# Optimization experiments

Hardware: AMD Instinct MI355X
Metric: run time of the kernel (lower is better)

The kernel has to match this reference:

```python
import jax, jax.numpy as jnp
import numpy as np

SIGMA = 1.0

def _pairwise_sqdist(x, y):
    # x: [N,3], y: [M,3] -> [N,M] squared distances via gram expansion
    xx = jnp.sum(x * x, axis=-1)[:, None]
    yy = jnp.sum(y * y, axis=-1)[None, :]
    xy = x @ y.T
    return jnp.maximum(xx + yy - 2.0 * xy, 0.0)

def _cauchy(d2, sigma):
    return 1.0 / (1.0 + d2 / (sigma * sigma))

def setup_inputs() -> dict:
    key = jax.random.key(0)
    k1, k2, k3, k4 = jax.random.split(key, 4)
    V, N, M = 4096, 8192, 8192
    src_vertices = jax.random.normal(k1, (V, 3), dtype=jnp.float32)
    tar_normals = jax.random.normal(k2, (M, 3), dtype=jnp.float32)
    tar_centers = jax.random.normal(k3, (M, 3), dtype=jnp.float32)
    src_indices = jax.random.randint(k4, (N, 3), 0, V)
    return {"src_vertices": src_vertices, "tar_normals": tar_normals,
            "tar_centers": tar_centers, "src_indices": src_indices}

def reference(src_vertices, tar_normals, tar_centers, src_indices):
    # Gather triangle vertices: [N,3(verts),3(xyz)]
    tris = src_vertices[src_indices]
    a, b, c = tris[:, 0, :], tris[:, 1, :], tris[:, 2, :]
    normals = 0.5 * jnp.cross(a - b, c - b)        # [N,3]
    centers = tris.sum(axis=1) / 3.0               # [N,3]

    # Currents energy with cauchy kernel K(x,y) = 1/(1 + |x-y|^2/sigma^2)
    K_ss = _cauchy(_pairwise_sqdist(centers, centers), SIGMA)      # [N,N]
    K_st = _cauchy(_pairwise_sqdist(centers, tar_centers), SIGMA)  # [N,M]
    K_tt = _cauchy(_pairwise_sqdist(tar_centers, tar_centers), SIGMA)  # [M,M]

    e_ss = jnp.sum(K_ss * (normals @ normals.T))
    e_st = jnp.sum(K_st * (normals @ tar_normals.T))
    e_tt = jnp.sum(K_tt * (tar_normals @ tar_normals.T))
    return e_ss - 2.0 * e_st + e_tt
```

## Files before the change

kernel.cpp:

```cpp
#include <hip/hip_runtime.h>

typedef short bf16x8 __attribute__((ext_vector_type(8)));
typedef float f32x16 __attribute__((ext_vector_type(16)));

static __device__ __forceinline__ unsigned short f2bf(float x) {
    unsigned u = __builtin_bit_cast(unsigned, x);
    unsigned r = (u + 0x7FFFu + ((u >> 16) & 1u)) >> 16;
    return (unsigned short)r;
}
static __device__ __forceinline__ float bf2f(unsigned short h) {
    unsigned u = (unsigned)h << 16;
    return __builtin_bit_cast(float, u);
}

__global__ void dc_pack(const float* __restrict__ verts,
                        const float* __restrict__ tnorm,
                        const float* __restrict__ tcent,
                        const int* __restrict__ idx,
                        unsigned short* __restrict__ ws,
                        float* __restrict__ out,
                        int N, int M) {
    int p = blockIdx.x * blockDim.x + threadIdx.x;
    if (p == 0) out[0] = 0.0f;
    int P = N + M;
    if (p >= P) return;

    float cx, cy, cz, nx, ny, nz;
    if (p < N) {
        int i0 = idx[3 * p + 0], i1 = idx[3 * p + 1], i2 = idx[3 * p + 2];
        float ax = verts[3 * i0], ay = verts[3 * i0 + 1], az = verts[3 * i0 + 2];
        float bx = verts[3 * i1], by = verts[3 * i1 + 1], bz = verts[3 * i1 + 2];
        float qx = verts[3 * i2], qy = verts[3 * i2 + 1], qz = verts[3 * i2 + 2];
        float ux = ax - bx, uy = ay - by, uz = az - bz;
        float vx = qx - bx, vy = qy - by, vz = qz - bz;
        nx = 0.5f * (uy * vz - uz * vy);
        ny = 0.5f * (uz * vx - ux * vz);
        nz = 0.5f * (ux * vy - uy * vx);
        cx = (ax + bx + qx) * (1.0f / 3.0f);
        cy = (ay + by + qy) * (1.0f / 3.0f);
        cz = (az + bz + qz) * (1.0f / 3.0f);
    } else {
        int t = p - N;
        cx = tcent[3 * t]; cy = tcent[3 * t + 1]; cz = tcent[3 * t + 2];
        nx = -tnorm[3 * t]; ny = -tnorm[3 * t + 1]; nz = -tnorm[3 * t + 2];
    }

    unsigned short chx = f2bf(cx), chy = f2bf(cy), chz = f2bf(cz);
    unsigned short clx = f2bf(cx - bf2f(chx));
    unsigned short cly = f2bf(cy - bf2f(chy));
    unsigned short clz = f2bf(cz - bf2f(chz));
    unsigned short nhx = f2bf(nx), nhy = f2bf(ny), nhz = f2bf(nz);
    unsigned short nlx = f2bf(nx - bf2f(nhx));
    unsigned short nly = f2bf(ny - bf2f(nhy));
    unsigned short nlz = f2bf(nz - bf2f(nhz));
    float ex = bf2f(chx) + bf2f(clx);
    float ey = bf2f(chy) + bf2f(cly);
    float ez = bf2f(chz) + bf2f(clz);
    float s = ex * ex + ey * ey + ez * ez;
    unsigned short sh = f2bf(s), sl = f2bf(s - bf2f(sh));
    unsigned short m2hx = f2bf(-2.0f * bf2f(chx)), m2hy = f2bf(-2.0f * bf2f(chy)), m2hz = f2bf(-2.0f * bf2f(chz));
    unsigned short m2lx = f2bf(-2.0f * bf2f(clx)), m2ly = f2bf(-2.0f * bf2f(cly)), m2lz = f2bf(-2.0f * bf2f(clz));
    const unsigned short one = 0x3F80;

    __align__(16) unsigned short A1v[16] = {
        m2hx, m2hy, m2hz,  m2hx, m2hy, m2hz,  m2lx, m2ly, m2lz,
        sh, sl,  one, one,  one,  0, 0 };
    __align__(16) unsigned short B1v[16] = {
        chx, chy, chz,  clx, cly, clz,  chx, chy, chz,
        one, one,  sh, sl,  one,  0, 0 };
    __align__(16) unsigned short A2v[16] = {
        nhx, nhy, nhz,  nhx, nhy, nhz,  nlx, nly, nlz,
        0, 0, 0, 0, 0, 0, 0 };
    __align__(16) unsigned short B2v[16] = {
        nhx, nhy, nhz,  nlx, nly, nlz,  nhx, nhy, nhz,
        0, 0, 0, 0, 0, 0, 0 };

    size_t arr = (size_t)P * 16;
    unsigned short* A1 = ws;
    unsigned short* B1 = ws + arr;
    unsigned short* A2 = ws + 2 * arr;
    unsigned short* B2 = ws + 3 * arr;

    int tile = p >> 5, m = p & 31;
    size_t lo = ((size_t)tile * 64 + m) * 8;
    size_t hi = lo + 32 * 8;

    *(uint4*)(A1 + lo) = *(const uint4*)&A1v[0];
    *(uint4*)(A1 + hi) = *(const uint4*)&A1v[8];
    *(uint4*)(B1 + lo) = *(const uint4*)&B1v[0];
    *(uint4*)(B1 + hi) = *(const uint4*)&B1v[8];
    *(uint4*)(A2 + lo) = *(const uint4*)&A2v[0];
    *(uint4*)(A2 + hi) = *(const uint4*)&A2v[8];
    *(uint4*)(B2 + lo) = *(const uint4*)&B2v[0];
    *(uint4*)(B2 + hi) = *(const uint4*)&B2v[8];
}

__global__ __launch_bounds__(256, 4) void dc_pair_mfma(
    const unsigned short* __restrict__ ws, float* __restrict__ out,
    int P, int nJpw) {
    __shared__ float wsum[4];

    size_t arr = (size_t)P * 16;
    const unsigned short* A1 = ws;
    const unsigned short* B1 = ws + arr;
    const unsigned short* A2 = ws + 2 * arr;
    const unsigned short* B2 = ws + 3 * arr;

    int tid = threadIdx.x;
    int lane = tid & 63, wv = tid >> 6;
    int I = blockIdx.x >> 1;
    int j0 = (blockIdx.x & 1) * (4 * nJpw) + wv * nJpw;

    bf16x8 a1 = *(const bf16x8*)(A1 + ((size_t)I * 64 + lane) * 8);
    bf16x8 a2 = *(const bf16x8*)(A2 + ((size_t)I * 64 + lane) * 8);

    f32x16 zero = {0.f,0.f,0.f,0.f,0.f,0.f,0.f,0.f,0.f,0.f,0.f,0.f,0.f,0.f,0.f,0.f};
    f32x16 part = zero;

    const unsigned short* pb1 = B1 + ((size_t)j0 * 64 + lane) * 8;
    const unsigned short* pb2 = B2 + ((size_t)j0 * 64 + lane) * 8;

#pragma unroll 2
    for (int j = 0; j < nJpw; ++j) {
        bf16x8 b1 = *(const bf16x8*)pb1;
        bf16x8 b2 = *(const bf16x8*)pb2;
        pb1 += 512; pb2 += 512;
        f32x16 d1 = __builtin_amdgcn_mfma_f32_32x32x16_bf16(a1, b1, zero, 0, 0, 0);
        f32x16 d2 = __builtin_amdgcn_mfma_f32_32x32x16_bf16(a2, b2, zero, 0, 0, 0);
#pragma unroll
        for (int r = 0; r < 16; ++r)
            part[r] = fmaf(__builtin_amdgcn_rcpf(d1[r]), d2[r], part[r]);
    }

    float s = 0.0f;
#pragma unroll
    for (int r = 0; r < 16; ++r) s += part[r];
#pragma unroll
    for (int off = 32; off > 0; off >>= 1) s += __shfl_down(s, off, 64);
    if (lane == 0) wsum[wv] = s;
    __syncthreads();
    if (tid == 0) {
        float t = wsum[0] + wsum[1] + wsum[2] + wsum[3];
        atomicAdd(out, t);
    }
}

extern "C" void kernel_launch(void* const* d_in, const int* in_sizes, int n_in,
                              void* d_out, int out_size, void* d_ws, size_t ws_size,
                              hipStream_t stream) {
    const float* verts = (const float*)d_in[0];
    const float* tnorm = (const float*)d_in[1];
    const float* tcent = (const float*)d_in[2];
    const int*   sidx  = (const int*)d_in[3];

    int M = in_sizes[1] / 3;
    int N = in_sizes[3] / 3;
    int P = N + M;

    unsigned short* ws = (unsigned short*)d_ws;
    float* out = (float*)d_out;

    int bblocks = (P + 255) / 256;
    dc_pack<<<bblocks, 256, 0, stream>>>(verts, tnorm, tcent, sidx, ws, out, N, M);

    int nI = P / 32;
    int nJpw = nI / 8;
    dc_pair_mfma<<<nI * 2, 256, 0, stream>>>(ws, out, P, nJpw);
}
```

Before: 99.49 us.

## Exploit kernel symmetry: compute upper-triangular 64x64 super-tiles with balanced persistent waves

Uses the symmetry of the combined pairwise energy matrix to evaluate only the upper-triangular 64x64 super-tile pairs. Off-diagonal contributions are doubled, and diagonal sub-blocks get half weight so the doubled sum stays exact. The triangular work list is split evenly across a fixed grid of 1280 blocks x 4 waves, with a closed-form sqrt mapping from linear index to tile row. Each loaded A/B fragment now feeds more MFMAs, which should roughly halve MFMA and reciprocal work, at the cost of branchy diagonal handling and per-wave index setup.

Result: no change. 99.76 us (+0.3%).

```diff
diff --git a/kernel.cpp b/kernel.cpp
--- a/kernel.cpp
+++ b/kernel.cpp
@@ -1,4 +1,5 @@
 #include <hip/hip_runtime.h>
+#include <math.h>
 
 typedef short bf16x8 __attribute__((ext_vector_type(8)));
 typedef float f32x16 __attribute__((ext_vector_type(16)));
@@ -95,11 +96,23 @@
     *(uint4*)(B2 + hi) = *(const uint4*)&B2v[8];
 }
 
-__global__ __launch_bounds__(256, 4) void dc_pair_mfma(
+static __device__ __forceinline__ void acc_full(f32x16& part, const f32x16& d1, const f32x16& d2) {
+#pragma unroll
+    for (int r = 0; r < 16; ++r)
+        part[r] = fmaf(__builtin_amdgcn_rcpf(d1[r]), d2[r], part[r]);
+}
+static __device__ __forceinline__ void acc_half(f32x16& part, const f32x16& d1, const f32x16& d2) {
+#pragma unroll
+    for (int r = 0; r < 16; ++r)
+        part[r] = fmaf(0.5f * __builtin_amdgcn_rcpf(d1[r]), d2[r], part[r]);
+}
+
+__global__ __launch_bounds__(256, 5) void dc_pair_mfma(
     const unsigned short* __restrict__ ws, float* __restrict__ out,
-    int P, int nJpw) {
+    int P, int W, int Tt) {
     __shared__ float wsum[4];
 
+    const int nS = P >> 6;
     size_t arr = (size_t)P * 16;
     const unsigned short* A1 = ws;
     const unsigned short* B1 = ws + arr;
@@ -108,33 +121,68 @@
 
     int tid = threadIdx.x;
     int lane = tid & 63, wv = tid >> 6;
-    int I = blockIdx.x >> 1;
-    int j0 = (blockIdx.x & 1) * (4 * nJpw) + wv * nJpw;
-
-    bf16x8 a1 = *(const bf16x8*)(A1 + ((size_t)I * 64 + lane) * 8);
-    bf16x8 a2 = *(const bf16x8*)(A2 + ((size_t)I * 64 + lane) * 8);
-
-    f32x16 zero = {0.f,0.f,0.f,0.f,0.f,0.f,0.f,0.f,0.f,0.f,0.f,0.f,0.f,0.f,0.f,0.f};
+    int wgid = blockIdx.x * 4 + wv;
+
+    int q = Tt / W, r = Tt % W;
+    int start = wgid * q + (wgid < r ? wgid : r);
+    int cnt = q + (wgid < r ? 1 : 0);
+
+    double dn = (double)(2 * nS + 1);
+    int S = (int)((dn - sqrt(dn * dn - 8.0 * (double)start)) * 0.5);
+    if (S >= nS) S = nS - 1;
+    if (S < 0) S = 0;
+#define CUM(s) ((s) * nS - ((s) * ((s) - 1)) / 2)
+    while (S > 0 && CUM(S) > start) --S;
+    while (CUM(S + 1) <= start) ++S;
+    int Ti = S + (start - CUM(S));
+#undef CUM
+
+    const f32x16 zero = {0.f,0.f,0.f,0.f,0.f,0.f,0.f,0.f,0.f,0.f,0.f,0.f,0.f,0.f,0.f,0.f};
     f32x16 part = zero;
 
-    const unsigned short* pb1 = B1 + ((size_t)j0 * 64 + lane) * 8;
-    const unsigned short* pb2 = B2 + ((size_t)j0 * 64 + lane) * 8;
-
-#pragma unroll 2
-    for (int j = 0; j < nJpw; ++j) {
-        bf16x8 b1 = *(const bf16x8*)pb1;
-        bf16x8 b2 = *(const bf16x8*)pb2;
-        pb1 += 512; pb2 += 512;
-        f32x16 d1 = __builtin_amdgcn_mfma_f32_32x32x16_bf16(a1, b1, zero, 0, 0, 0);
-        f32x16 d2 = __builtin_amdgcn_mfma_f32_32x32x16_bf16(a2, b2, zero, 0, 0, 0);
-#pragma unroll
-        for (int r = 0; r < 16; ++r)
-            part[r] = fmaf(__builtin_amdgcn_rcpf(d1[r]), d2[r], part[r]);
+    bf16x8 a1_0 = *(const bf16x8*)(A1 + ((size_t)(2 * S) * 64 + lane) * 8);
+    bf16x8 a1_1 = *(const bf16x8*)(A1 + ((size_t)(2 * S + 1) * 64 + lane) * 8);
+    bf16x8 a2_0 = *(const bf16x8*)(A2 + ((size_t)(2 * S) * 64 + lane) * 8);
+    bf16x8 a2_1 = *(const bf16x8*)(A2 + ((size_t)(2 * S + 1) * 64 + lane) * 8);
+
+    for (int it = 0; it < cnt; ++it) {
+        int J = 2 * Ti;
+        bf16x8 b1_0 = *(const bf16x8*)(B1 + ((size_t)J * 64 + lane) * 8);
+        bf16x8 b1_1 = *(const bf16x8*)(B1 + ((size_t)(J + 1) * 64 + lane) * 8);
+        bf16x8 b2_0 = *(const bf16x8*)(B2 + ((size_t)J * 64 + lane) * 8);
+        bf16x8 b2_1 = *(const bf16x8*)(B2 + ((size_t)(J + 1) * 64 + lane) * 8);
+        bool diag = (Ti == S);
+
+        f32x16 d1, d2;
+        d1 = __builtin_amdgcn_mfma_f32_32x32x16_bf16(a1_0, b1_0, zero, 0, 0, 0);
+        d2 = __builtin_amdgcn_mfma_f32_32x32x16_bf16(a2_0, b2_0, zero, 0, 0, 0);
+        if (diag) acc_half(part, d1, d2); else acc_full(part, d1, d2);
+        d1 = __builtin_amdgcn_mfma_f32_32x32x16_bf16(a1_0, b1_1, zero, 0, 0, 0);
+        d2 = __builtin_amdgcn_mfma_f32_32x32x16_bf16(a2_0, b2_1, zero, 0, 0, 0);
+        acc_full(part, d1, d2);
+        if (!diag) {
+            d1 = __builtin_amdgcn_mfma_f32_32x32x16_bf16(a1_1, b1_0, zero, 0, 0, 0);
+            d2 = __builtin_amdgcn_mfma_f32_32x32x16_bf16(a2_1, b2_0, zero, 0, 0, 0);
+            acc_full(part, d1, d2);
+        }
+        d1 = __builtin_amdgcn_mfma_f32_32x32x16_bf16(a1_1, b1_1, zero, 0, 0, 0);
+        d2 = __builtin_amdgcn_mfma_f32_32x32x16_bf16(a2_1, b2_1, zero, 0, 0, 0);
+        if (diag) acc_half(part, d1, d2); else acc_full(part, d1, d2);
+
+        ++Ti;
+        if (Ti >= nS && (it + 1) < cnt) {
+            ++S; Ti = S;
+            a1_0 = *(const bf16x8*)(A1 + ((size_t)(2 * S) * 64 + lane) * 8);
+            a1_1 = *(const bf16x8*)(A1 + ((size_t)(2 * S + 1) * 64 + lane) * 8);
+            a2_0 = *(const bf16x8*)(A2 + ((size_t)(2 * S) * 64 + lane) * 8);
+            a2_1 = *(const bf16x8*)(A2 + ((size_t)(2 * S + 1) * 64 + lane) * 8);
+        }
     }
 
     float s = 0.0f;
 #pragma unroll
-    for (int r = 0; r < 16; ++r) s += part[r];
+    for (int rr = 0; rr < 16; ++rr) s += part[rr];
+    s *= 2.0f;
 #pragma unroll
     for (int off = 32; off > 0; off >>= 1) s += __shfl_down(s, off, 64);
     if (lane == 0) wsum[wv] = s;
@@ -163,7 +211,9 @@
     int bblocks = (P + 255) / 256;
     dc_pack<<<bblocks, 256, 0, stream>>>(verts, tnorm, tcent, sidx, ws, out, N, M);
 
-    int nI = P / 32;
-    int nJpw = nI / 8;
-    dc_pair_mfma<<<nI * 2, 256, 0, stream>>>(ws, out, P, nJpw);
-}
+    int nS = P >> 6;
+    int Tt = nS * (nS + 1) / 2;
+    int nBlocks = 1280;
+    int W = nBlocks * 4;
+    dc_pair_mfma<<<nBlocks, 256, 0, stream>>>(ws, out, P, W, Tt);
+}
```

## Exploit kernel symmetry with circulant tile pairing and batched reciprocals

Applied to the files above, without the earlier changes.

Because the pairwise sum is symmetric, each row tile I now visits only the tile offsets d from 0 to nT/2 (wrapping modulo nT), splits that range into ten chunks spread over waves, halves the weight on the diagonal and antipodal offsets, and doubles the total. This roughly halves the MFMA and epilogue work. The epilogue also merges four 1/d1 terms into one reciprocal via products of denominators, which cuts rcp instructions but risks overflow or precision loss in those products. The chunk constants (26 and 25 tiles) are hard-coded for nT=512, and occupancy is raised to 5 blocks per SIMD.

After: 90.42 us. -9.1%, faster.

```diff
diff --git a/kernel.cpp b/kernel.cpp
--- a/kernel.cpp
+++ b/kernel.cpp
@@ -95,11 +95,29 @@
     *(uint4*)(B2 + hi) = *(const uint4*)&B2v[8];
 }
 
-__global__ __launch_bounds__(256, 4) void dc_pair_mfma(
-    const unsigned short* __restrict__ ws, float* __restrict__ out,
-    int P, int nJpw) {
+template <bool HALF>
+static __device__ __forceinline__ void acc4(float4& part, const f32x16& d1, const f32x16& d2) {
+#pragma unroll
+    for (int g = 0; g < 4; ++g) {
+        const int r = 4 * g;
+        float p01 = d1[r] * d1[r + 1];
+        float p23 = d1[r + 2] * d1[r + 3];
+        float n01 = fmaf(d2[r], d1[r + 1], d2[r + 1] * d1[r]);
+        float n23 = fmaf(d2[r + 2], d1[r + 3], d2[r + 3] * d1[r + 2]);
+        float t   = p01 * p23;
+        float num = fmaf(n01, p23, n23 * p01);
+        float rk  = __builtin_amdgcn_rcpf(t);
+        if (HALF) rk *= 0.5f;
+        (&part.x)[g] = fmaf(num, rk, (&part.x)[g]);
+    }
+}
+
+__global__ __launch_bounds__(256, 5) void dc_pair_mfma(
+    const unsigned short* __restrict__ ws, float* __restrict__ out, int P) {
     __shared__ float wsum[4];
 
+    const int nT = P >> 5;
+    const int half = nT >> 1;
     size_t arr = (size_t)P * 16;
     const unsigned short* A1 = ws;
     const unsigned short* B1 = ws + arr;
@@ -108,33 +126,33 @@
 
     int tid = threadIdx.x;
     int lane = tid & 63, wv = tid >> 6;
-    int I = blockIdx.x >> 1;
-    int j0 = (blockIdx.x & 1) * (4 * nJpw) + wv * nJpw;
+    int g = blockIdx.x * 4 + wv;
+    int I = g / 10;
+    int c = g - 10 * I;
+
+    int st  = c * 26 - (c > 7 ? c - 7 : 0);
+    int len = 26 - (c >= 7 ? 1 : 0);
 
     bf16x8 a1 = *(const bf16x8*)(A1 + ((size_t)I * 64 + lane) * 8);
     bf16x8 a2 = *(const bf16x8*)(A2 + ((size_t)I * 64 + lane) * 8);
 
-    f32x16 zero = {0.f,0.f,0.f,0.f,0.f,0.f,0.f,0.f,0.f,0.f,0.f,0.f,0.f,0.f,0.f,0.f};
-    f32x16 part = zero;
-
-    const unsigned short* pb1 = B1 + ((size_t)j0 * 64 + lane) * 8;
-    const unsigned short* pb2 = B2 + ((size_t)j0 * 64 + lane) * 8;
+    const f32x16 zero = {0.f,0.f,0.f,0.f,0.f,0.f,0.f,0.f,0.f,0.f,0.f,0.f,0.f,0.f,0.f,0.f};
+    float4 part = make_float4(0.f, 0.f, 0.f, 0.f);
 
 #pragma unroll 2
-    for (int j = 0; j < nJpw; ++j) {
-        bf16x8 b1 = *(const bf16x8*)pb1;
-        bf16x8 b2 = *(const bf16x8*)pb2;
-        pb1 += 512; pb2 += 512;
+    for (int it = 0; it < len; ++it) {
+        int d = st + it;
+        int j = I + d;
+        int jm = (j >= nT) ? j - nT : j;
+        const bf16x8 b1 = *(const bf16x8*)(B1 + ((size_t)jm * 64 + lane) * 8);
+        const bf16x8 b2 = *(const bf16x8*)(B2 + ((size_t)jm * 64 + lane) * 8);
         f32x16 d1 = __builtin_amdgcn_mfma_f32_32x32x16_bf16(a1, b1, zero, 0, 0, 0);
         f32x16 d2 = __builtin_amdgcn_mfma_f32_32x32x16_bf16(a2, b2, zero, 0, 0, 0);
-#pragma unroll
-        for (int r = 0; r < 16; ++r)
-            part[r] = fmaf(__builtin_amdgcn_rcpf(d1[r]), d2[r], part[r]);
+        if (d == 0 || d == half) acc4<true>(part, d1, d2);
+        else                     acc4<false>(part, d1, d2);
     }
 
-    float s = 0.0f;
-#pragma unroll
-    for (int r = 0; r < 16; ++r) s += part[r];
+    float s = (part.x + part.y + part.z + part.w) * 2.0f;
 #pragma unroll
     for (int off = 32; off > 0; off >>= 1) s += __shfl_down(s, off, 64);
     if (lane == 0) wsum[wv] = s;
@@ -163,7 +181,7 @@
     int bblocks = (P + 255) / 256;
     dc_pack<<<bblocks, 256, 0, stream>>>(verts, tnorm, tcent, sidx, ws, out, N, M);
 
-    int nI = P / 32;
-    int nJpw = nI / 8;
-    dc_pair_mfma<<<nI * 2, 256, 0, stream>>>(ws, out, P, nJpw);
+    int nT = P >> 5;
+    int nBlocks = (nT * 10) / 4;
+    dc_pair_mfma<<<nBlocks, 256, 0, stream>>>(ws, out, P);
 }
```
